# Kernel tuning notes

Hardware: AMD Instinct MI355X
Metric: run time of the kernel (lower is better)

## Reference

```python
import jax, jax.numpy as jnp
import numpy as np

NUM_NODES = 100000
NODE_CH = 3     # node_fiber_channels (degree-0)
EDGE_CH = 3     # edge_fiber_channels (degree-0)
MID = 32        # RadialProfile hidden dim (NVIDIA SE3-Transformer default)
VALUE_CH = 1    # fiber_out channels // channels_div = 3 // 2
KQ_CH = 1       # key/query channels (match value fiber on shared degrees)
BATCH = 64


def setup_inputs() -> dict:
    key = jax.random.key(0)
    ks = jax.random.split(key, 8)
    s = 0.1
    return {
        "input_data": jax.random.normal(ks[0], (BATCH, 3, NUM_NODES, 3), jnp.float32),
        # RadialProfile MLP: edge_feats -> MID -> MID -> (VALUE_CH+KQ_CH)*NODE_CH (last layer no bias)
        "W1": jax.random.normal(ks[1], (EDGE_CH, MID), jnp.float32) * s,
        "b1": jnp.zeros((MID,), jnp.float32),
        "W2": jax.random.normal(ks[2], (MID, MID), jnp.float32) * s,
        "b2": jnp.zeros((MID,), jnp.float32),
        "W3": jax.random.normal(ks[3], (MID, (VALUE_CH + KQ_CH) * NODE_CH), jnp.float32) * s,
        # LinearSE3 query (deg 0): (KQ_CH, NODE_CH)
        "Wq": jax.random.normal(ks[4], (KQ_CH, NODE_CH), jnp.float32) * s,
        # LinearSE3 project after cat-skip: (NODE_CH, VALUE_CH + NODE_CH)
        "Wp": jax.random.normal(ks[5], (NODE_CH, VALUE_CH + NODE_CH), jnp.float32) * s,
    }


def reference(input_data, W1, b1, W2, b2, W3, Wq, Wp):
    B, C, N, _ = input_data.shape
    node = input_data[:, 0]               # (B, N, 3) degree-0 node feats
    edge = input_data[:, 2]               # (B, E=N, 3) degree-0 edge feats
    src = jnp.arange(N)                   # ring graph: i -> (i+1) % N
    dst = (src + 1) % N

    # ConvSE3 deg0->deg0 (to_key_value): radial MLP on invariant edge feats
    # produces a per-edge (out_ch, in_ch) matrix applied to source-node feats.
    h = jax.nn.relu(edge @ W1 + b1)
    h = jax.nn.relu(h @ W2 + b2)
    R = (h @ W3).reshape(B, N, VALUE_CH + KQ_CH, NODE_CH)      # (B,E,2,3)
    kv = jnp.einsum('beoc,bec->beo', R, node[:, src])          # (B,E,2)
    value = kv[..., 0]                                         # chunk: value first
    key_e = kv[..., 1]                                         # key second

    # LinearSE3 query at nodes
    q = jnp.einsum('bnc,kc->bnk', node, Wq)[..., 0]            # (B,N)

    # AttentionSE3: dot(key, query[dst]) / sqrt(key feats), softmax over
    # incoming edges of each destination node (ring: exactly one per node).
    logits = key_e * q[:, dst] / jnp.sqrt(jnp.float32(KQ_CH))  # (B,E)
    m = jnp.full((B, N), -jnp.inf, logits.dtype).at[:, dst].max(logits)
    ex = jnp.exp(logits - m[:, dst])
    denom = jnp.zeros((B, N), logits.dtype).at[:, dst].add(ex)
    alpha = ex / denom[:, dst]
    z = jnp.zeros((B, N), logits.dtype).at[:, dst].add(alpha * value)  # (B,N)

    # aggregate_residual 'cat' ([attn_out, node]) then LinearSE3 project
    feat = jnp.concatenate([z[..., None], node], axis=-1)      # (B,N,4)
    out0 = jnp.einsum('bnc,oc->bno', feat, Wp)                 # (B,N,3)

    # channels 1 and 2 pass through unchanged
    return input_data.at[:, 0].set(out0)
```

## Files before the change

kernel.cpp:

```cpp
#include <hip/hip_runtime.h>

#define N_NODES 100000
#define BATCH   64
#define MID     32
#define LSTRIDE 80
#define WLDS    (64 * LSTRIDE + 512)
#define TOTAL   (BATCH * N_NODES)

typedef __attribute__((ext_vector_type(2))) __fp16 h2v;
typedef _Float16 __attribute__((ext_vector_type(8))) f16x8;
typedef float __attribute__((ext_vector_type(4))) f32x4;
typedef float __attribute__((ext_vector_type(2))) f32x2;

union H2U  { h2v h; unsigned int u; };
union U4H8 { uint4 u; f16x8 h; };

struct __attribute__((packed, aligned(4))) F4u { f32x4 v; };
struct __attribute__((packed, aligned(4))) F2u { f32x2 v; };

__global__ void prep_weights(const float* __restrict__ W1, const float* __restrict__ b1,
                             const float* __restrict__ W2, const float* __restrict__ W3,
                             uint4* __restrict__ wf, unsigned int* __restrict__ aux) {
    int t = threadIdx.x;
    if (t < 128) {
        int grp = t >> 6, l = t & 63;
        int j = (l & 15) + 16 * grp, k0 = (l >> 4) * 8;
        unsigned int pk[4];
#pragma unroll
        for (int m = 0; m < 4; ++m) {
            H2U a; a.h = __builtin_amdgcn_cvt_pkrtz(W2[(k0 + 2*m) * MID + j],
                                                    W2[(k0 + 2*m + 1) * MID + j]);
            pk[m] = a.u;
        }
        wf[t] = make_uint4(pk[0], pk[1], pk[2], pk[3]);
    } else if (t < 192) {
        int l = t & 63;
        int c = l & 15, q4 = l >> 4;
        unsigned int pk[4];
#pragma unroll
        for (int mp = 0; mp < 4; ++mp) {
            int jb = (mp < 2) ? (4*q4 + 2*mp) : (16 + 4*q4 + 2*(mp - 2));
            float x0 = (c < 3) ? W3[jb * 6 + c] : 0.f;
            float x1 = (c < 3) ? W3[(jb + 1) * 6 + c] : 0.f;
            H2U a; a.h = __builtin_amdgcn_cvt_pkrtz(x0, x1);
            pk[mp] = a.u;
        }
        wf[128 + l] = make_uint4(pk[0], pk[1], pk[2], pk[3]);
    } else if (t < 240) {
        int i = t - 192;
        int k = i >> 4, m = i & 15;
        H2U a; a.h = __builtin_amdgcn_cvt_pkrtz(W1[k * MID + 2*m], W1[k * MID + 2*m + 1]);
        aux[i] = a.u;
    } else {
        int m = t - 240;
        H2U a; a.h = __builtin_amdgcn_cvt_pkrtz(b1[2*m], b1[2*m + 1]);
        aux[48 + m] = a.u;
    }
}

__global__ __launch_bounds__(256) void xattn_kernel(
    const float* __restrict__ in,
    const unsigned int* __restrict__ aux,
    const float* __restrict__ b2,
    const uint4* __restrict__ wf,
    const float* __restrict__ Wp,
    float* __restrict__ out)
{
    __shared__ __attribute__((aligned(16))) char ldsbuf[4 * WLDS];
    int tid  = threadIdx.x;
    int lane = tid & 63;
    int wave = tid >> 6;
    char* L  = ldsbuf + wave * WLDS;
    char* ZB = L + 64 * LSTRIDE;

    int idx = blockIdx.x * 256 + tid;
    int b = idx / N_NODES;
    int n = idx - b * N_NODES;
    bool last = (idx == TOTAL - 1);
    bool btail = (n == N_NODES - 1);

    const float* inb  = in  + (size_t)b * (3u * N_NODES * 3u);
    float*       outb = out + (size_t)b * (3u * N_NODES * 3u);

    f32x4 ndv = ((const F4u*)(inb + (size_t)n * 3))->v;
    f32x4 c1v = ((const F4u*)(inb + (size_t)N_NODES * 3 + (size_t)n * 3))->v;
    f32x4 edv;
    const float* e_ptr = inb + (size_t)2 * N_NODES * 3 + (size_t)n * 3;
    if (!last) edv = ((const F4u*)e_ptr)->v;
    else       edv = (f32x4){e_ptr[0], e_ptr[1], e_ptr[2], 0.f};

    float qn0 = ndv.x, qn1 = ndv.y, qn2 = ndv.z;

    {
        float* o1p = outb + (size_t)N_NODES * 3 + (size_t)n * 3;
        ((F4u*)o1p)->v = c1v;
        float* o2p = outb + (size_t)2 * N_NODES * 3 + (size_t)n * 3;
        if (!btail) ((F4u*)o2p)->v = edv;
        else { o2p[0] = edv.x; o2p[1] = edv.y; o2p[2] = edv.z; }
    }

    H2U s0_, s1_, s2_;
    s0_.h = __builtin_amdgcn_cvt_pkrtz(qn0, qn1);
    s1_.h = __builtin_amdgcn_cvt_pkrtz(qn2, edv.x);
    s2_.h = __builtin_amdgcn_cvt_pkrtz(edv.y, edv.z);
    unsigned int t0 = __shfl_up(s0_.u, 1);
    unsigned int t1 = __shfl_up(s1_.u, 1);
    unsigned int t2 = __shfl_up(s2_.u, 1);
    if (lane == 0 || n == 0) {
        int p = (n == 0) ? (N_NODES - 1) : (n - 1);
        const float* np_ = inb + (size_t)p * 3;
        const float* epp = inb + ((size_t)2 * N_NODES + p) * 3;
        H2U a, bb, c;
        a.h  = __builtin_amdgcn_cvt_pkrtz(np_[0], np_[1]);
        bb.h = __builtin_amdgcn_cvt_pkrtz(np_[2], epp[0]);
        c.h  = __builtin_amdgcn_cvt_pkrtz(epp[1], epp[2]);
        t0 = a.u; t1 = bb.u; t2 = c.u;
    }
    H2U u0, u1, u2; u0.u = t0; u1.u = t1; u2.u = t2;
    float pp0 = (float)u0.h[0], pp1 = (float)u0.h[1], pp2 = (float)u1.h[0];
    h2v eh0 = {u1.h[1], u1.h[1]};
    h2v eh1 = {u2.h[0], u2.h[0]};
    h2v eh2 = {u2.h[1], u2.h[1]};

    h2v zz = {(__fp16)0.0f, (__fp16)0.0f};
    unsigned int hp[16];
#pragma unroll
    for (int m = 0; m < 16; ++m) {
        H2U acc, w0, w1_, w2_;
        acc.u = aux[48 + m];
        w0.u  = aux[m];
        w1_.u = aux[16 + m];
        w2_.u = aux[32 + m];
        acc.h = eh0 * w0.h + acc.h;
        acc.h = eh1 * w1_.h + acc.h;
        acc.h = eh2 * w2_.h + acc.h;
        acc.h = __builtin_elementwise_max(acc.h, zz);
        hp[m] = acc.u;
    }
    {
        uint4* row = (uint4*)(L + lane * LSTRIDE);
        row[0] = make_uint4(hp[0],  hp[1],  hp[2],  hp[3]);
        row[1] = make_uint4(hp[4],  hp[5],  hp[6],  hp[7]);
        row[2] = make_uint4(hp[8],  hp[9],  hp[10], hp[11]);
        row[3] = make_uint4(hp[12], hp[13], hp[14], hp[15]);
    }

    int r16 = lane & 15;
    int q4  = lane >> 4;
    U4H8 wb20; wb20.u = wf[lane];
    U4H8 wb21; wb21.u = wf[64 + lane];
    U4H8 wb3;  wb3.u  = wf[128 + lane];
    f32x4 bi0 = *(const f32x4*)(b2 + 4*q4);
    f32x4 bi1 = *(const f32x4*)(b2 + 16 + 4*q4);

#pragma unroll
    for (int pt = 0; pt < 4; ++pt) {
        U4H8 hB; hB.u = *(const uint4*)(L + (pt*16 + r16) * LSTRIDE + q4 * 16);
        f32x4 acc0 = bi0;
        f32x4 acc1 = bi1;
        acc0 = __builtin_amdgcn_mfma_f32_16x16x32_f16(wb20.h, hB.h, acc0, 0, 0, 0);
        acc1 = __builtin_amdgcn_mfma_f32_16x16x32_f16(wb21.h, hB.h, acc1, 0, 0, 0);

        H2U g0, g1, g2, g3;
        g0.h = __builtin_elementwise_max(__builtin_amdgcn_cvt_pkrtz(acc0[0], acc0[1]), zz);
        g1.h = __builtin_elementwise_max(__builtin_amdgcn_cvt_pkrtz(acc0[2], acc0[3]), zz);
        g2.h = __builtin_elementwise_max(__builtin_amdgcn_cvt_pkrtz(acc1[0], acc1[1]), zz);
        g3.h = __builtin_elementwise_max(__builtin_amdgcn_cvt_pkrtz(acc1[2], acc1[3]), zz);
        U4H8 b3f; b3f.u = make_uint4(g0.u, g1.u, g2.u, g3.u);

        f32x4 c3 = __builtin_amdgcn_mfma_f32_16x16x32_f16(wb3.h, b3f.h,
                                                          (f32x4){0.f,0.f,0.f,0.f}, 0, 0, 0);

        if (q4 == 0) {
            H2U za; za.h = __builtin_amdgcn_cvt_pkrtz(c3[0], c3[1]);
            H2U zb; zb.h = __builtin_amdgcn_cvt_pkrtz(c3[2], 0.f);
            *(uint2*)(ZB + (pt*16 + r16) * 8) = make_uint2(za.u, zb.u);
        }
    }

    uint2 zr = *(const uint2*)(ZB + lane * 8);
    H2U za, zb; za.u = zr.x; zb.u = zr.y;
    float z = fmaf((float)za.h[0], pp0,
              fmaf((float)za.h[1], pp1, (float)zb.h[0] * pp2));

    float vo[3];
#pragma unroll
    for (int o = 0; o < 3; ++o) {
        float v = Wp[o*4 + 0] * z;
        v = fmaf(Wp[o*4 + 1], qn0, v);
        v = fmaf(Wp[o*4 + 2], qn1, v);
        v = fmaf(Wp[o*4 + 3], qn2, v);
        vo[o] = v;
    }
    float* o0 = outb + (size_t)n * 3;
    ((F2u*)o0)->v = (f32x2){vo[0], vo[1]};
    o0[2] = vo[2];
}

extern "C" void kernel_launch(void* const* d_in, const int* in_sizes, int n_in,
                              void* d_out, int out_size, void* d_ws, size_t ws_size,
                              hipStream_t stream) {
    const float* in = (const float*)d_in[0];
    const float* W1 = (const float*)d_in[1];
    const float* b1 = (const float*)d_in[2];
    const float* W2 = (const float*)d_in[3];
    const float* b2 = (const float*)d_in[4];
    const float* W3 = (const float*)d_in[5];
    const float* Wp = (const float*)d_in[7];
    float* out = (float*)d_out;

    uint4* wf = (uint4*)d_ws;
    unsigned int* aux = (unsigned int*)(wf + 192);
    hipLaunchKernelGGL(prep_weights, dim3(1), dim3(256), 0, stream, W1, b1, W2, W3, wf, aux);

    int blocks = TOTAL / 256;
    hipLaunchKernelGGL(xattn_kernel, dim3(blocks), dim3(256), 0, stream,
                       in, aux, b2, wf, Wp, out);
}
```

Before: 95.55 us.

## Process four nodes per thread with aligned 16-byte vector loads and stores

Each thread now handles four consecutive nodes, so its 12-float slices of every channel are 16-byte aligned and move with three full vector loads and stores instead of unaligned packed accesses. The predecessor of nodes 1-3 comes from the thread's own registers, and only node 0 needs a cross-lane shuffle. The radial MLP/MFMA pipeline loops four times per thread over the same per-wave LDS buffer, and the grid shrinks by four. This gives fewer threads and more serial work per wave, which may reduce latency hiding. The grid of TOTAL/1024 also assumes the per-batch node count is a multiple of four.

```diff
diff --git a/kernel.cpp b/kernel.cpp
--- a/kernel.cpp
+++ b/kernel.cpp
@@ -6,17 +6,14 @@
 #define LSTRIDE 80
 #define WLDS    (64 * LSTRIDE + 512)
 #define TOTAL   (BATCH * N_NODES)
+#define CHF     (N_NODES * 3)
 
 typedef __attribute__((ext_vector_type(2))) __fp16 h2v;
 typedef _Float16 __attribute__((ext_vector_type(8))) f16x8;
 typedef float __attribute__((ext_vector_type(4))) f32x4;
-typedef float __attribute__((ext_vector_type(2))) f32x2;
 
 union H2U  { h2v h; unsigned int u; };
 union U4H8 { uint4 u; f16x8 h; };
-
-struct __attribute__((packed, aligned(4))) F4u { f32x4 v; };
-struct __attribute__((packed, aligned(4))) F2u { f32x2 v; };
 
 __global__ void prep_weights(const float* __restrict__ W1, const float* __restrict__ b1,
                              const float* __restrict__ W2, const float* __restrict__ W3,
@@ -73,76 +70,49 @@
     char* L  = ldsbuf + wave * WLDS;
     char* ZB = L + 64 * LSTRIDE;
 
-    int idx = blockIdx.x * 256 + tid;
-    int b = idx / N_NODES;
-    int n = idx - b * N_NODES;
-    bool last = (idx == TOTAL - 1);
-    bool btail = (n == N_NODES - 1);
-
-    const float* inb  = in  + (size_t)b * (3u * N_NODES * 3u);
-    float*       outb = out + (size_t)b * (3u * N_NODES * 3u);
-
-    f32x4 ndv = ((const F4u*)(inb + (size_t)n * 3))->v;
-    f32x4 c1v = ((const F4u*)(inb + (size_t)N_NODES * 3 + (size_t)n * 3))->v;
-    f32x4 edv;
-    const float* e_ptr = inb + (size_t)2 * N_NODES * 3 + (size_t)n * 3;
-    if (!last) edv = ((const F4u*)e_ptr)->v;
-    else       edv = (f32x4){e_ptr[0], e_ptr[1], e_ptr[2], 0.f};
-
-    float qn0 = ndv.x, qn1 = ndv.y, qn2 = ndv.z;
+    int gt   = blockIdx.x * 256 + tid;
+    int idx4 = gt * 4;
+    int b  = idx4 / N_NODES;
+    int n0 = idx4 - b * N_NODES;
+
+    const float* inb  = in  + (size_t)b * (3u * CHF / 3u) * 3u;
+    float*       outb = out + (size_t)b * 3u * CHF;
+
+    const f32x4* npv = (const f32x4*)(inb + (size_t)n0 * 3);
+    f32x4 nda = npv[0], ndb = npv[1], ndc = npv[2];
+    const f32x4* c1pv = (const f32x4*)(inb + CHF + (size_t)n0 * 3);
+    f32x4 c1a = c1pv[0], c1b = c1pv[1], c1c = c1pv[2];
+    const f32x4* edpv = (const f32x4*)(inb + 2 * CHF + (size_t)n0 * 3);
+    f32x4 eda = edpv[0], edb = edpv[1], edc = edpv[2];
 
     {
-        float* o1p = outb + (size_t)N_NODES * 3 + (size_t)n * 3;
-        ((F4u*)o1p)->v = c1v;
-        float* o2p = outb + (size_t)2 * N_NODES * 3 + (size_t)n * 3;
-        if (!btail) ((F4u*)o2p)->v = edv;
-        else { o2p[0] = edv.x; o2p[1] = edv.y; o2p[2] = edv.z; }
-    }
+        f32x4* o1 = (f32x4*)(outb + CHF + (size_t)n0 * 3);
+        o1[0] = c1a; o1[1] = c1b; o1[2] = c1c;
+        f32x4* o2 = (f32x4*)(outb + 2 * CHF + (size_t)n0 * 3);
+        o2[0] = eda; o2[1] = edb; o2[2] = edc;
+    }
+
+    float nd[12] = {nda[0],nda[1],nda[2],nda[3], ndb[0],ndb[1],ndb[2],ndb[3], ndc[0],ndc[1],ndc[2],ndc[3]};
+    float eg[12] = {eda[0],eda[1],eda[2],eda[3], edb[0],edb[1],edb[2],edb[3], edc[0],edc[1],edc[2],edc[3]};
 
     H2U s0_, s1_, s2_;
-    s0_.h = __builtin_amdgcn_cvt_pkrtz(qn0, qn1);
-    s1_.h = __builtin_amdgcn_cvt_pkrtz(qn2, edv.x);
-    s2_.h = __builtin_amdgcn_cvt_pkrtz(edv.y, edv.z);
+    s0_.h = __builtin_amdgcn_cvt_pkrtz(nd[9], nd[10]);
+    s1_.h = __builtin_amdgcn_cvt_pkrtz(nd[11], eg[9]);
+    s2_.h = __builtin_amdgcn_cvt_pkrtz(eg[10], eg[11]);
     unsigned int t0 = __shfl_up(s0_.u, 1);
     unsigned int t1 = __shfl_up(s1_.u, 1);
     unsigned int t2 = __shfl_up(s2_.u, 1);
-    if (lane == 0 || n == 0) {
-        int p = (n == 0) ? (N_NODES - 1) : (n - 1);
+    float p0n0, p0n1, p0n2, p0e0, p0e1, p0e2;
+    if (lane == 0 || n0 == 0) {
+        int p = (n0 == 0) ? (N_NODES - 1) : (n0 - 1);
         const float* np_ = inb + (size_t)p * 3;
-        const float* epp = inb + ((size_t)2 * N_NODES + p) * 3;
-        H2U a, bb, c;
-        a.h  = __builtin_amdgcn_cvt_pkrtz(np_[0], np_[1]);
-        bb.h = __builtin_amdgcn_cvt_pkrtz(np_[2], epp[0]);
-        c.h  = __builtin_amdgcn_cvt_pkrtz(epp[1], epp[2]);
-        t0 = a.u; t1 = bb.u; t2 = c.u;
-    }
-    H2U u0, u1, u2; u0.u = t0; u1.u = t1; u2.u = t2;
-    float pp0 = (float)u0.h[0], pp1 = (float)u0.h[1], pp2 = (float)u1.h[0];
-    h2v eh0 = {u1.h[1], u1.h[1]};
-    h2v eh1 = {u2.h[0], u2.h[0]};
-    h2v eh2 = {u2.h[1], u2.h[1]};
-
-    h2v zz = {(__fp16)0.0f, (__fp16)0.0f};
-    unsigned int hp[16];
-#pragma unroll
-    for (int m = 0; m < 16; ++m) {
-        H2U acc, w0, w1_, w2_;
-        acc.u = aux[48 + m];
-        w0.u  = aux[m];
-        w1_.u = aux[16 + m];
-        w2_.u = aux[32 + m];
-        acc.h = eh0 * w0.h + acc.h;
-        acc.h = eh1 * w1_.h + acc.h;
-        acc.h = eh2 * w2_.h + acc.h;
-        acc.h = __builtin_elementwise_max(acc.h, zz);
-        hp[m] = acc.u;
-    }
-    {
-        uint4* row = (uint4*)(L + lane * LSTRIDE);
-        row[0] = make_uint4(hp[0],  hp[1],  hp[2],  hp[3]);
-        row[1] = make_uint4(hp[4],  hp[5],  hp[6],  hp[7]);
-        row[2] = make_uint4(hp[8],  hp[9],  hp[10], hp[11]);
-        row[3] = make_uint4(hp[12], hp[13], hp[14], hp[15]);
+        const float* epp = inb + 2 * CHF + (size_t)p * 3;
+        p0n0 = np_[0]; p0n1 = np_[1]; p0n2 = np_[2];
+        p0e0 = epp[0]; p0e1 = epp[1]; p0e2 = epp[2];
+    } else {
+        H2U u0, u1, u2; u0.u = t0; u1.u = t1; u2.u = t2;
+        p0n0 = (float)u0.h[0]; p0n1 = (float)u0.h[1]; p0n2 = (float)u1.h[0];
+        p0e0 = (float)u1.h[1]; p0e1 = (float)u2.h[0]; p0e2 = (float)u2.h[1];
     }
 
     int r16 = lane & 15;
@@ -152,49 +122,88 @@
     U4H8 wb3;  wb3.u  = wf[128 + lane];
     f32x4 bi0 = *(const f32x4*)(b2 + 4*q4);
     f32x4 bi1 = *(const f32x4*)(b2 + 16 + 4*q4);
-
-#pragma unroll
-    for (int pt = 0; pt < 4; ++pt) {
-        U4H8 hB; hB.u = *(const uint4*)(L + (pt*16 + r16) * LSTRIDE + q4 * 16);
-        f32x4 acc0 = bi0;
-        f32x4 acc1 = bi1;
-        acc0 = __builtin_amdgcn_mfma_f32_16x16x32_f16(wb20.h, hB.h, acc0, 0, 0, 0);
-        acc1 = __builtin_amdgcn_mfma_f32_16x16x32_f16(wb21.h, hB.h, acc1, 0, 0, 0);
-
-        H2U g0, g1, g2, g3;
-        g0.h = __builtin_elementwise_max(__builtin_amdgcn_cvt_pkrtz(acc0[0], acc0[1]), zz);
-        g1.h = __builtin_elementwise_max(__builtin_amdgcn_cvt_pkrtz(acc0[2], acc0[3]), zz);
-        g2.h = __builtin_elementwise_max(__builtin_amdgcn_cvt_pkrtz(acc1[0], acc1[1]), zz);
-        g3.h = __builtin_elementwise_max(__builtin_amdgcn_cvt_pkrtz(acc1[2], acc1[3]), zz);
-        U4H8 b3f; b3f.u = make_uint4(g0.u, g1.u, g2.u, g3.u);
-
-        f32x4 c3 = __builtin_amdgcn_mfma_f32_16x16x32_f16(wb3.h, b3f.h,
-                                                          (f32x4){0.f,0.f,0.f,0.f}, 0, 0, 0);
-
-        if (q4 == 0) {
-            H2U za; za.h = __builtin_amdgcn_cvt_pkrtz(c3[0], c3[1]);
-            H2U zb; zb.h = __builtin_amdgcn_cvt_pkrtz(c3[2], 0.f);
-            *(uint2*)(ZB + (pt*16 + r16) * 8) = make_uint2(za.u, zb.u);
-        }
-    }
-
-    uint2 zr = *(const uint2*)(ZB + lane * 8);
-    H2U za, zb; za.u = zr.x; zb.u = zr.y;
-    float z = fmaf((float)za.h[0], pp0,
-              fmaf((float)za.h[1], pp1, (float)zb.h[0] * pp2));
-
-    float vo[3];
-#pragma unroll
-    for (int o = 0; o < 3; ++o) {
-        float v = Wp[o*4 + 0] * z;
-        v = fmaf(Wp[o*4 + 1], qn0, v);
-        v = fmaf(Wp[o*4 + 2], qn1, v);
-        v = fmaf(Wp[o*4 + 3], qn2, v);
-        vo[o] = v;
-    }
-    float* o0 = outb + (size_t)n * 3;
-    ((F2u*)o0)->v = (f32x2){vo[0], vo[1]};
-    o0[2] = vo[2];
+    h2v zz = {(__fp16)0.0f, (__fp16)0.0f};
+
+    float vo[12];
+
+#pragma unroll
+    for (int r = 0; r < 4; ++r) {
+        float pe0 = (r == 0) ? p0e0 : eg[3*(r-1) + 0];
+        float pe1 = (r == 0) ? p0e1 : eg[3*(r-1) + 1];
+        float pe2 = (r == 0) ? p0e2 : eg[3*(r-1) + 2];
+        float pn0 = (r == 0) ? p0n0 : nd[3*(r-1) + 0];
+        float pn1 = (r == 0) ? p0n1 : nd[3*(r-1) + 1];
+        float pn2 = (r == 0) ? p0n2 : nd[3*(r-1) + 2];
+
+        h2v eh0 = __builtin_amdgcn_cvt_pkrtz(pe0, pe0);
+        h2v eh1 = __builtin_amdgcn_cvt_pkrtz(pe1, pe1);
+        h2v eh2 = __builtin_amdgcn_cvt_pkrtz(pe2, pe2);
+        unsigned int hp[16];
+#pragma unroll
+        for (int m = 0; m < 16; ++m) {
+            H2U acc, w0, w1_, w2_;
+            acc.u = aux[48 + m];
+            w0.u  = aux[m];
+            w1_.u = aux[16 + m];
+            w2_.u = aux[32 + m];
+            acc.h = eh0 * w0.h + acc.h;
+            acc.h = eh1 * w1_.h + acc.h;
+            acc.h = eh2 * w2_.h + acc.h;
+            acc.h = __builtin_elementwise_max(acc.h, zz);
+            hp[m] = acc.u;
+        }
+        {
+            uint4* row = (uint4*)(L + lane * LSTRIDE);
+            row[0] = make_uint4(hp[0],  hp[1],  hp[2],  hp[3]);
+            row[1] = make_uint4(hp[4],  hp[5],  hp[6],  hp[7]);
+            row[2] = make_uint4(hp[8],  hp[9],  hp[10], hp[11]);
+            row[3] = make_uint4(hp[12], hp[13], hp[14], hp[15]);
+        }
+
+#pragma unroll
+        for (int pt = 0; pt < 4; ++pt) {
+            U4H8 hB; hB.u = *(const uint4*)(L + (pt*16 + r16) * LSTRIDE + q4 * 16);
+            f32x4 acc0 = bi0;
+            f32x4 acc1 = bi1;
+            acc0 = __builtin_amdgcn_mfma_f32_16x16x32_f16(wb20.h, hB.h, acc0, 0, 0, 0);
+            acc1 = __builtin_amdgcn_mfma_f32_16x16x32_f16(wb21.h, hB.h, acc1, 0, 0, 0);
+
+            H2U g0, g1, g2, g3;
+            g0.h = __builtin_elementwise_max(__builtin_amdgcn_cvt_pkrtz(acc0[0], acc0[1]), zz);
+            g1.h = __builtin_elementwise_max(__builtin_amdgcn_cvt_pkrtz(acc0[2], acc0[3]), zz);
+            g2.h = __builtin_elementwise_max(__builtin_amdgcn_cvt_pkrtz(acc1[0], acc1[1]), zz);
+            g3.h = __builtin_elementwise_max(__builtin_amdgcn_cvt_pkrtz(acc1[2], acc1[3]), zz);
+            U4H8 b3f; b3f.u = make_uint4(g0.u, g1.u, g2.u, g3.u);
+
+            f32x4 c3 = __builtin_amdgcn_mfma_f32_16x16x32_f16(wb3.h, b3f.h,
+                                                              (f32x4){0.f,0.f,0.f,0.f}, 0, 0, 0);
+            if (q4 == 0) {
+                H2U za; za.h = __builtin_amdgcn_cvt_pkrtz(c3[0], c3[1]);
+                H2U zb; zb.h = __builtin_amdgcn_cvt_pkrtz(c3[2], 0.f);
+                *(uint2*)(ZB + (pt*16 + r16) * 8) = make_uint2(za.u, zb.u);
+            }
+        }
+
+        uint2 zr = *(const uint2*)(ZB + lane * 8);
+        H2U za, zb; za.u = zr.x; zb.u = zr.y;
+        float z = fmaf((float)za.h[0], pn0,
+                  fmaf((float)za.h[1], pn1, (float)zb.h[0] * pn2));
+
+        float qn0 = nd[3*r + 0], qn1 = nd[3*r + 1], qn2 = nd[3*r + 2];
+#pragma unroll
+        for (int o = 0; o < 3; ++o) {
+            float v = Wp[o*4 + 0] * z;
+            v = fmaf(Wp[o*4 + 1], qn0, v);
+            v = fmaf(Wp[o*4 + 2], qn1, v);
+            v = fmaf(Wp[o*4 + 3], qn2, v);
+            vo[3*r + o] = v;
+        }
+    }
+
+    f32x4* o0 = (f32x4*)(outb + (size_t)n0 * 3);
+    o0[0] = (f32x4){vo[0], vo[1], vo[2],  vo[3]};
+    o0[1] = (f32x4){vo[4], vo[5], vo[6],  vo[7]};
+    o0[2] = (f32x4){vo[8], vo[9], vo[10], vo[11]};
 }
 
 extern "C" void kernel_launch(void* const* d_in, const int* in_sizes, int n_in,
@@ -213,7 +222,7 @@
     unsigned int* aux = (unsigned int*)(wf + 192);
     hipLaunchKernelGGL(prep_weights, dim3(1), dim3(256), 0, stream, W1, b1, W2, W3, wf, aux);
 
-    int blocks = TOTAL / 256;
+    int blocks = TOTAL / 1024;
     hipLaunchKernelGGL(xattn_kernel, dim3(blocks), dim3(256), 0, stream,
                        in, aux, b2, wf, Wp, out);
 }
```

After: 105.9 us. 1.11x slower.

## Split channel-1 passthrough into dedicated interleaved bulk-copy blocks

Applied to the files above, without the earlier changes.

The compute blocks no longer copy input channel 1 to the output. Separate copy blocks, interleaved every 11th block in the grid, move that channel with contiguous uint4 loads and stores, 8 per thread. Channel-1 traffic becomes fully coalesced 16-byte-aligned streaming instead of unaligned per-node 16-byte accesses, and the compute blocks do less work. The cost is extra block scheduling and more complex block-index remapping, and copy blocks still reserve the kernel's large static LDS allocation.

```diff
diff --git a/kernel.cpp b/kernel.cpp
--- a/kernel.cpp
+++ b/kernel.cpp
@@ -6,6 +6,12 @@
 #define LSTRIDE 80
 #define WLDS    (64 * LSTRIDE + 512)
 #define TOTAL   (BATCH * N_NODES)
+#define CHF     (N_NODES * 3)
+#define CH_U4   (CHF / 4)
+#define CPB     37
+#define NCOPY   (CPB * BATCH)
+#define NCOMP   (TOTAL / 256)
+#define NGRID   (NCOPY + NCOMP)
 
 typedef __attribute__((ext_vector_type(2))) __fp16 h2v;
 typedef _Float16 __attribute__((ext_vector_type(8))) f16x8;
@@ -68,33 +74,48 @@
 {
     __shared__ __attribute__((aligned(16))) char ldsbuf[4 * WLDS];
     int tid  = threadIdx.x;
+    int bidx = blockIdx.x;
+
+    if (bidx % 11 == 5 && (bidx / 11) < NCOPY) {
+        int cb    = bidx / 11;
+        int batch = cb / CPB;
+        int blk   = cb - batch * CPB;
+        const uint4* src = (const uint4*)(in  + (size_t)batch * 3 * CHF + CHF);
+        uint4*       dst = (uint4*)(out + (size_t)batch * 3 * CHF + CHF);
+        int base = blk * 2048 + tid;
+#pragma unroll
+        for (int k = 0; k < 8; ++k) {
+            int i = base + k * 256;
+            if (i < CH_U4) dst[i] = src[i];
+        }
+        return;
+    }
+
+    int cid  = bidx - min(NCOPY, (bidx + 5) / 11);
     int lane = tid & 63;
     int wave = tid >> 6;
     char* L  = ldsbuf + wave * WLDS;
     char* ZB = L + 64 * LSTRIDE;
 
-    int idx = blockIdx.x * 256 + tid;
+    int idx = cid * 256 + tid;
     int b = idx / N_NODES;
     int n = idx - b * N_NODES;
-    bool last = (idx == TOTAL - 1);
+    bool last  = (idx == TOTAL - 1);
     bool btail = (n == N_NODES - 1);
 
-    const float* inb  = in  + (size_t)b * (3u * N_NODES * 3u);
-    float*       outb = out + (size_t)b * (3u * N_NODES * 3u);
+    const float* inb  = in  + (size_t)b * 3 * CHF;
+    float*       outb = out + (size_t)b * 3 * CHF;
 
     f32x4 ndv = ((const F4u*)(inb + (size_t)n * 3))->v;
-    f32x4 c1v = ((const F4u*)(inb + (size_t)N_NODES * 3 + (size_t)n * 3))->v;
     f32x4 edv;
-    const float* e_ptr = inb + (size_t)2 * N_NODES * 3 + (size_t)n * 3;
+    const float* e_ptr = inb + (size_t)2 * CHF + (size_t)n * 3;
     if (!last) edv = ((const F4u*)e_ptr)->v;
     else       edv = (f32x4){e_ptr[0], e_ptr[1], e_ptr[2], 0.f};
 
     float qn0 = ndv.x, qn1 = ndv.y, qn2 = ndv.z;
 
     {
-        float* o1p = outb + (size_t)N_NODES * 3 + (size_t)n * 3;
-        ((F4u*)o1p)->v = c1v;
-        float* o2p = outb + (size_t)2 * N_NODES * 3 + (size_t)n * 3;
+        float* o2p = outb + (size_t)2 * CHF + (size_t)n * 3;
         if (!btail) ((F4u*)o2p)->v = edv;
         else { o2p[0] = edv.x; o2p[1] = edv.y; o2p[2] = edv.z; }
     }
@@ -109,7 +130,7 @@
     if (lane == 0 || n == 0) {
         int p = (n == 0) ? (N_NODES - 1) : (n - 1);
         const float* np_ = inb + (size_t)p * 3;
-        const float* epp = inb + ((size_t)2 * N_NODES + p) * 3;
+        const float* epp = inb + (size_t)2 * CHF + (size_t)p * 3;
         H2U a, bb, c;
         a.h  = __builtin_amdgcn_cvt_pkrtz(np_[0], np_[1]);
         bb.h = __builtin_amdgcn_cvt_pkrtz(np_[2], epp[0]);
@@ -213,7 +234,6 @@
     unsigned int* aux = (unsigned int*)(wf + 192);
     hipLaunchKernelGGL(prep_weights, dim3(1), dim3(256), 0, stream, W1, b1, W2, W3, wf, aux);
 
-    int blocks = TOTAL / 256;
-    hipLaunchKernelGGL(xattn_kernel, dim3(blocks), dim3(256), 0, stream,
+    hipLaunchKernelGGL(xattn_kernel, dim3(NGRID), dim3(256), 0, stream,
                        in, aux, b2, wf, Wp, out);
 }
```

Result: slower. 100.3 us (+4.9%).
